# Performance work log

Measured on AMD Instinct MI355X. Metric: run time of the kernel, lower is better.

The kernel has to match this reference:

```python
import jax, jax.numpy as jnp
import numpy as np

T, B, D, H = 512, 64, 256, 512


def setup_inputs() -> dict:
    key = jax.random.key(0)
    k1, k2, k3, k4 = jax.random.split(key, 4)
    x = jax.random.normal(k1, (T, B, D), dtype=jnp.float32)
    should_reset = jax.random.randint(k2, (T, B), 0, 2, dtype=jnp.int32)
    # Linear([x, h]) -> 4H gates, Haiku/PyTorch-style fan-in init scale
    scale = 1.0 / np.sqrt(D + H)
    W = jax.random.normal(k3, (D + H, 4 * H), dtype=jnp.float32) * scale
    b = jax.random.normal(k4, (4 * H,), dtype=jnp.float32) * scale
    return {"x": x, "should_reset": should_reset, "W": W, "b": b}


def reference(x, should_reset, W, b):
    """ResetLSTM forward (reverse=False). x:[T,B,D], should_reset:[T,B] -> [T,B,H]."""
    h0 = jnp.zeros((x.shape[1], H), dtype=x.dtype)
    c0 = jnp.zeros((x.shape[1], H), dtype=x.dtype)
    reset = should_reset.astype(x.dtype)[..., None]  # [T,B,1]

    def step(carry, inp):
        h, c = carry
        xt, rt = inp
        keep = 1.0 - rt
        h = h * keep
        c = c * keep
        gates = jnp.concatenate([xt, h], axis=-1) @ W + b  # [B,4H]
        i, g, f, o = jnp.split(gates, 4, axis=-1)
        f = jax.nn.sigmoid(f + 1.0)  # Haiku forget bias +1
        i = jax.nn.sigmoid(i)
        g = jnp.tanh(g)
        o = jax.nn.sigmoid(o)
        new_c = f * c + i * g
        new_h = o * jnp.tanh(new_c)
        return (new_h, new_c), new_h

    _, outputs = jax.lax.scan(step, (h0, c0), (x, reset))
    return outputs  # [T,B,H]
```

## Files before the change

kernel.cpp:

```cpp
#include <hip/hip_runtime.h>

#define TSTEPS 512
#define BATCH  64
#define DIN    256
#define HID    512
#define NCH    8
#define VR     512
#define NRB    16
#define NUB    32
#define NWG    512
#define NTHR   256
#define HSST   520
#define GST    67

typedef __attribute__((ext_vector_type(8))) _Float16 f16x8;
typedef __attribute__((ext_vector_type(4))) _Float16 f16x4;
typedef __attribute__((ext_vector_type(4))) float f32x4;
typedef __attribute__((ext_vector_type(2))) float f32x2;

#define MFMA16(A,B,C) __builtin_amdgcn_mfma_f32_16x16x32_f16(A,B,C,0,0,0)
#define ALDU32(p) __hip_atomic_load(const_cast<unsigned*>(p), __ATOMIC_RELAXED, __HIP_MEMORY_SCOPE_AGENT)
#define ASTU32(p,v) __hip_atomic_store((p), (v), __ATOMIC_RELAXED, __HIP_MEMORY_SCOPE_AGENT)

__device__ __forceinline__ float sigm(float x) { return 1.0f / (1.0f + __expf(-x)); }

__device__ __forceinline__ void gld16_cc(f16x8& d, const void* p) {
  asm volatile("global_load_dwordx4 %0, %1, off sc0 sc1" : "=v"(d) : "v"(p));
}

__global__ void conv_x(const float* __restrict__ x, _Float16* __restrict__ xh, int n4) {
  int i = blockIdx.x * 256 + threadIdx.x;
  if (i >= n4) return;
  float4 v = reinterpret_cast<const float4*>(x)[i];
  f16x4 o;
  o[0] = (_Float16)v.x; o[1] = (_Float16)v.y; o[2] = (_Float16)v.z; o[3] = (_Float16)v.w;
  *reinterpret_cast<f16x4*>(xh + (size_t)i * 4) = o;
}

__global__ void w_prep(const float* __restrict__ W,
                       _Float16* __restrict__ WxT, _Float16* __restrict__ WhT) {
  int idx = blockIdx.x * 256 + threadIdx.x;
  if (idx < NUB * 64 * 256) {
    int k = idx & 255, cc = (idx >> 8) & 63, ub = idx >> 14;
    int unit = cc >> 2, g = cc & 3;
    int gcol = g * HID + ub * 16 + unit;
    WxT[idx] = (_Float16)W[k * 2048 + gcol];
  } else if (idx < NUB * 64 * 256 + NUB * 64 * 512) {
    int j = idx - NUB * 64 * 256;
    int k = j & 511, cc = (j >> 9) & 63, ub = j >> 15;
    int unit = cc >> 2, g = cc & 3;
    int gcol = g * HID + ub * 16 + unit;
    WhT[j] = (_Float16)W[(DIN + k) * 2048 + gcol];
  }
}

__global__ void seg_prep(const int* __restrict__ rst, int* __restrict__ tS,
                         int* __restrict__ segLen, int* __restrict__ maxLenB) {
  __shared__ int sMax[NRB];
  const int b = threadIdx.x;
  if (b < NRB) sMax[b] = 0;
  __syncthreads();
  int cut[NCH + 1];
  cut[0] = 0; cut[NCH] = TSTEPS;
  for (int c = 1; c < NCH; ++c) {
    int t = c * 64;
    while (t < TSTEPS && rst[t * BATCH + b] == 0) ++t;
    cut[c] = t;
  }
  for (int c = 1; c < NCH; ++c) if (cut[c] < cut[c - 1]) cut[c] = cut[c - 1];
  for (int c = 0; c < NCH; ++c) {
    int vr = c * 64 + b;
    tS[vr] = cut[c];
    int L = cut[c + 1] - cut[c];
    segLen[vr] = L;
    atomicMax(&sMax[c * 2 + (b >> 5)], L);
  }
  __syncthreads();
  if (b < NRB) maxLenB[b] = sMax[b];
}

__global__ void __launch_bounds__(NTHR, 2)
lstm_persistent(const _Float16* __restrict__ xh,
                const int* __restrict__ rst,
                const float* __restrict__ bias,
                float* __restrict__ out,
                unsigned long long* __restrict__ hb,
                unsigned* __restrict__ flags,
                const _Float16* __restrict__ WxT,
                const _Float16* __restrict__ WhT,
                const int* __restrict__ tS,
                const int* __restrict__ segLen,
                const int* __restrict__ maxLenB) {
  __shared__ _Float16 hS[32 * HSST];
  __shared__ float gateS[32 * GST];
  __shared__ float biasS[64];

  const int tid = threadIdx.x, wg = blockIdx.x;
  const int rb = wg >> 5, ub = wg & 31;
  const int vr0 = rb * 32;
  const int lane = tid & 63, wave = tid >> 6;
  const int colA = lane & 15, klo = (lane >> 4) * 8;

  f16x8 wx[8], wh[16];
  {
    const _Float16* px = WxT + ((size_t)ub * 64 + wave * 16 + colA) * 256 + klo;
    const _Float16* ph = WhT + ((size_t)ub * 64 + wave * 16 + colA) * 512 + klo;
#pragma unroll
    for (int ch = 0; ch < 8; ++ch) wx[ch] = *(const f16x8*)(px + ch * 32);
#pragma unroll
    for (int ch = 0; ch < 16; ++ch) wh[ch] = *(const f16x8*)(ph + ch * 32);
  }
  if (tid < 64) {
    int unit = tid >> 2, g = tid & 3;
    biasS[tid] = bias[g * HID + ub * 16 + unit];
  }

  int tSr0 = tS[vr0 + colA];
  int tSr1 = tS[vr0 + 16 + colA];

  const int crow = tid & 31, p = tid >> 5;
  const int vrc = vr0 + crow, bc = vrc & 63;
  const int tSc_ = tS[vrc], lenc_ = segLen[vrc];
  const int ML = maxLenB[rb];
  float cA = 0.f, cB = 0.f;

  __syncthreads();
  float bA[4], bB[4];
#pragma unroll
  for (int g = 0; g < 4; ++g) { bA[g] = biasS[8 * p + g]; bB[g] = biasS[8 * p + 4 + g]; }

  const int srow = tid >> 3, ss = tid & 7;

  for (int k = 0; k < ML; ++k) {
    f32x4 acc0 = {0.f, 0.f, 0.f, 0.f}, acc1 = {0.f, 0.f, 0.f, 0.f};
    {
      int t0 = tSr0 + k; if (t0 > TSTEPS - 1) t0 = TSTEPS - 1;
      int t1 = tSr1 + k; if (t1 > TSTEPS - 1) t1 = TSTEPS - 1;
      const int b0 = (vr0 + colA) & 63, b1 = (vr0 + 16 + colA) & 63;
      const _Float16* x0 = xh + ((size_t)t0 * BATCH + b0) * DIN + klo;
      const _Float16* x1 = xh + ((size_t)t1 * BATCH + b1) * DIN + klo;
#pragma unroll
      for (int ch = 0; ch < 8; ++ch) {
        f16x8 a0 = *(const f16x8*)(x0 + ch * 32);
        f16x8 a1 = *(const f16x8*)(x1 + ch * 32);
        acc0 = MFMA16(a0, wx[ch], acc0);
        acc1 = MFMA16(a1, wx[ch], acc1);
      }
    }

    if (k) {
      if (tid < NUB) {
        const unsigned tgt = (unsigned)k;
        while (ALDU32(flags + (rb * NUB + tid) * 16) < tgt) __builtin_amdgcn_s_sleep(1);
      }
      __syncthreads();
      asm volatile("" ::: "memory");

      {
        const char* hbase = (const char*)hb
            + (((size_t)(k & 1) * (VR * 128) + (size_t)(vr0 + srow) * 128) << 3)
            + ss * 16;
        f16x8 hq[8];
#pragma unroll
        for (int j = 0; j < 8; ++j) gld16_cc(hq[j], hbase + j * 128);
        asm volatile("s_waitcnt vmcnt(0)" ::: "memory");
        __builtin_amdgcn_sched_barrier(0);
#pragma unroll
        for (int j = 0; j < 8; ++j)
          *(f16x8*)&hS[srow * HSST + ss * 8 + j * 64] = hq[j];
      }
      __syncthreads();

#pragma unroll
      for (int ch = 0; ch < 16; ++ch) {
        f16x8 a0 = *(const f16x8*)&hS[colA * HSST + ch * 32 + klo];
        f16x8 a1 = *(const f16x8*)&hS[(16 + colA) * HSST + ch * 32 + klo];
        acc0 = MFMA16(a0, wh[ch], acc0);
        acc1 = MFMA16(a1, wh[ch], acc1);
      }
    }

#pragma unroll
    for (int rr = 0; rr < 4; ++rr) {
      int row0 = (lane >> 4) * 4 + rr;
      gateS[row0 * GST + wave * 16 + colA]        = acc0[rr];
      gateS[(16 + row0) * GST + wave * 16 + colA] = acc1[rr];
    }

    float hn0, hn1;
    {
      int kidx = tSc_ + k + 1; if (kidx > TSTEPS - 1) kidx = TSTEPS - 1;
      float keep = 1.0f - (float)rst[kidx * BATCH + bc];
      const float* g = &gateS[crow * GST + 8 * p];
      float i0 = sigm(g[0] + bA[0]);
      float t0 = tanhf(g[1] + bA[1]);
      float f0 = sigm(g[2] + bA[2] + 1.0f);
      float o0 = sigm(g[3] + bA[3]);
      float i1 = sigm(g[4] + bB[0]);
      float t1 = tanhf(g[5] + bB[1]);
      float f1 = sigm(g[6] + bB[2] + 1.0f);
      float o1 = sigm(g[7] + bB[3]);
      float cn0 = f0 * cA + i0 * t0, cn1 = f1 * cB + i1 * t1;
      hn0 = o0 * tanhf(cn0); hn1 = o1 * tanhf(cn1);
      cA = cn0 * keep; cB = cn1 * keep;
      if (k + 1 < ML) {
        union { _Float16 f[2]; unsigned u; } cv;
        cv.f[0] = (_Float16)(hn0 * keep);
        cv.f[1] = (_Float16)(hn1 * keep);
        unsigned* hb32 = (unsigned*)(hb + (size_t)((k + 1) & 1) * (VR * 128) + (size_t)vrc * 128);
        ASTU32(hb32 + ub * 8 + p, cv.u);
      }
    }

    __syncthreads();
    if (k + 1 < ML && tid == 0) ASTU32(flags + wg * 16, (unsigned)(k + 1));

    if (k < lenc_) {
      f32x2 o2 = {hn0, hn1};
      *(f32x2*)&out[((size_t)(tSc_ + k) * BATCH + bc) * HID + ub * 16 + 2 * p] = o2;
    }
  }
}

extern "C" void kernel_launch(void* const* d_in, const int* in_sizes, int n_in,
                              void* d_out, int out_size, void* d_ws, size_t ws_size,
                              hipStream_t stream) {
  const float* x   = (const float*)d_in[0];
  const int*   rst = (const int*)d_in[1];
  const float* W   = (const float*)d_in[2];
  const float* b   = (const float*)d_in[3];
  float* out = (float*)d_out;
  char* ws = (char*)d_ws;

  unsigned*           flags  = (unsigned*)(ws + 0);
  int*                tSp    = (int*)(ws + 32768);
  int*                segLen = (int*)(ws + 34816);
  int*                maxLenB= (int*)(ws + 36864);
  unsigned long long* hb     = (unsigned long long*)(ws + 40960);
  _Float16*           xh     = (_Float16*)(ws + 40960 + 1048576);
  _Float16*           WxT    = (_Float16*)(ws + 40960 + 1048576 + 16777216);
  _Float16*           WhT    = (_Float16*)(ws + 40960 + 1048576 + 16777216 + 1048576);

  hipMemsetAsync(ws, 0, 32768, stream);

  int n4 = TSTEPS * BATCH * DIN / 4;
  hipLaunchKernelGGL(conv_x, dim3(n4 / 256), dim3(256), 0, stream, x, xh, n4);
  hipLaunchKernelGGL(w_prep, dim3(6144), dim3(256), 0, stream, W, WxT, WhT);
  hipLaunchKernelGGL(seg_prep, dim3(1), dim3(64), 0, stream, rst, tSp, segLen, maxLenB);

  hipLaunchKernelGGL(lstm_persistent, dim3(NWG), dim3(NTHR), 0, stream,
                     xh, rst, b, out, hb, flags, WxT, WhT, tSp, segLen, maxLenB);
}
```

Measured before the change: 505.7 us.

## Balance reset-segment split, remap workgroups by XCC, use L2-scope h exchange

Segment cutting now binary-searches the smallest maximum chunk length, so each batch row's 8 chunks are balanced and the number of sequential steps (ML) can shrink. Workgroups are renumbered so the 32 unit-blocks sharing a row-block are strided by 16. At startup each workgroup records its XCC id; if all its partners share an XCC, the hidden-state exchange uses sc0 (L2-coherent) loads and stores instead of system-coherent ones, which cuts per-step communication latency. This adds a startup handshake and depends on the hardware dispatching the workgroups onto the same XCC, otherwise it falls back to the old path.

```diff
diff --git a/kernel.cpp b/kernel.cpp
--- a/kernel.cpp
+++ b/kernel.cpp
@@ -26,6 +26,12 @@
 
 __device__ __forceinline__ void gld16_cc(f16x8& d, const void* p) {
   asm volatile("global_load_dwordx4 %0, %1, off sc0 sc1" : "=v"(d) : "v"(p));
+}
+__device__ __forceinline__ void gld16_l2(f16x8& d, const void* p) {
+  asm volatile("global_load_dwordx4 %0, %1, off sc0" : "=v"(d) : "v"(p));
+}
+__device__ __forceinline__ void gld16_pin(f16x8& d, const void* p) {
+  asm volatile("global_load_dwordx4 %0, %1, off" : "=v"(d) : "v"(p));
 }
 
 __global__ void conv_x(const float* __restrict__ x, _Float16* __restrict__ xh, int n4) {
@@ -60,20 +66,34 @@
   const int b = threadIdx.x;
   if (b < NRB) sMax[b] = 0;
   __syncthreads();
-  int cut[NCH + 1];
-  cut[0] = 0; cut[NCH] = TSTEPS;
-  for (int c = 1; c < NCH; ++c) {
-    int t = c * 64;
-    while (t < TSTEPS && rst[t * BATCH + b] == 0) ++t;
-    cut[c] = t;
-  }
-  for (int c = 1; c < NCH; ++c) if (cut[c] < cut[c - 1]) cut[c] = cut[c - 1];
+  int lo = (TSTEPS + NCH - 1) / NCH, hi = TSTEPS;
+  while (lo < hi) {
+    int L = (lo + hi) >> 1;
+    int pos = 0; bool ok = false;
+    for (int s = 0; s < NCH; ++s) {
+      int target = pos + L;
+      if (target >= TSTEPS) { ok = true; break; }
+      int t = target;
+      while (t > pos && rst[t * BATCH + b] == 0) --t;
+      if (t == pos) break;
+      pos = t;
+    }
+    if (ok) hi = L; else lo = L + 1;
+  }
+  const int L = lo;
+  int pos = 0;
   for (int c = 0; c < NCH; ++c) {
+    int start = pos, end = pos;
+    if (pos < TSTEPS) {
+      int target = pos + L;
+      if (target >= TSTEPS) end = TSTEPS;
+      else { int t = target; while (t > pos && rst[t * BATCH + b] == 0) --t; end = t; }
+      pos = end;
+    }
     int vr = c * 64 + b;
-    tS[vr] = cut[c];
-    int L = cut[c + 1] - cut[c];
-    segLen[vr] = L;
-    atomicMax(&sMax[c * 2 + (b >> 5)], L);
+    tS[vr] = start;
+    segLen[vr] = end - start;
+    atomicMax(&sMax[c * 2 + (b >> 5)], end - start);
   }
   __syncthreads();
   if (b < NRB) maxLenB[b] = sMax[b];
@@ -86,6 +106,7 @@
                 float* __restrict__ out,
                 unsigned long long* __restrict__ hb,
                 unsigned* __restrict__ flags,
+                unsigned* __restrict__ xccb,
                 const _Float16* __restrict__ WxT,
                 const _Float16* __restrict__ WhT,
                 const int* __restrict__ tS,
@@ -94,21 +115,40 @@
   __shared__ _Float16 hS[32 * HSST];
   __shared__ float gateS[32 * GST];
   __shared__ float biasS[64];
+  __shared__ int uniformS;
 
   const int tid = threadIdx.x, wg = blockIdx.x;
-  const int rb = wg >> 5, ub = wg & 31;
+  const int ub = wg >> 4;
+  const int rb = ((wg & 7) << 1) | ((wg >> 3) & 1);
+  const int wgbase = wg & 15;
   const int vr0 = rb * 32;
   const int lane = tid & 63, wave = tid >> 6;
   const int colA = lane & 15, klo = (lane >> 4) * 8;
+
+  unsigned myxcc;
+  asm volatile("s_getreg_b32 %0, hwreg(HW_REG_XCC_ID)" : "=s"(myxcc));
+  if (tid == 0) {
+    uniformS = 1;
+    ASTU32(xccb + wg * 16, 0x100u | (myxcc & 0xffu));
+  }
+  __syncthreads();
+  if (tid < NUB) {
+    int mwg = (tid << 4) | wgbase;
+    unsigned v;
+    do { v = ALDU32(xccb + mwg * 16); if (!v) __builtin_amdgcn_s_sleep(1); } while (!v);
+    if ((v & 0xffu) != (myxcc & 0xffu)) uniformS = 0;
+  }
 
   f16x8 wx[8], wh[16];
   {
     const _Float16* px = WxT + ((size_t)ub * 64 + wave * 16 + colA) * 256 + klo;
     const _Float16* ph = WhT + ((size_t)ub * 64 + wave * 16 + colA) * 512 + klo;
 #pragma unroll
-    for (int ch = 0; ch < 8; ++ch) wx[ch] = *(const f16x8*)(px + ch * 32);
-#pragma unroll
-    for (int ch = 0; ch < 16; ++ch) wh[ch] = *(const f16x8*)(ph + ch * 32);
+    for (int ch = 0; ch < 8; ++ch) gld16_pin(wx[ch], px + ch * 32);
+#pragma unroll
+    for (int ch = 0; ch < 16; ++ch) gld16_pin(wh[ch], ph + ch * 32);
+    asm volatile("s_waitcnt vmcnt(0)" ::: "memory");
+    __builtin_amdgcn_sched_barrier(0);
   }
   if (tid < 64) {
     int unit = tid >> 2, g = tid & 3;
@@ -125,6 +165,7 @@
   float cA = 0.f, cB = 0.f;
 
   __syncthreads();
+  const bool useL2 = (uniformS != 0);
   float bA[4], bB[4];
 #pragma unroll
   for (int g = 0; g < 4; ++g) { bA[g] = biasS[8 * p + g]; bB[g] = biasS[8 * p + 4 + g]; }
@@ -151,7 +192,8 @@
     if (k) {
       if (tid < NUB) {
         const unsigned tgt = (unsigned)k;
-        while (ALDU32(flags + (rb * NUB + tid) * 16) < tgt) __builtin_amdgcn_s_sleep(1);
+        while (ALDU32(flags + ((tid << 4) | wgbase) * 16) < tgt)
+          __builtin_amdgcn_s_sleep(1);
       }
       __syncthreads();
       asm volatile("" ::: "memory");
@@ -161,8 +203,13 @@
             + (((size_t)(k & 1) * (VR * 128) + (size_t)(vr0 + srow) * 128) << 3)
             + ss * 16;
         f16x8 hq[8];
-#pragma unroll
-        for (int j = 0; j < 8; ++j) gld16_cc(hq[j], hbase + j * 128);
+        if (useL2) {
+#pragma unroll
+          for (int j = 0; j < 8; ++j) gld16_l2(hq[j], hbase + j * 128);
+        } else {
+#pragma unroll
+          for (int j = 0; j < 8; ++j) gld16_cc(hq[j], hbase + j * 128);
+        }
         asm volatile("s_waitcnt vmcnt(0)" ::: "memory");
         __builtin_amdgcn_sched_barrier(0);
 #pragma unroll
@@ -207,8 +254,12 @@
         union { _Float16 f[2]; unsigned u; } cv;
         cv.f[0] = (_Float16)(hn0 * keep);
         cv.f[1] = (_Float16)(hn1 * keep);
-        unsigned* hb32 = (unsigned*)(hb + (size_t)((k + 1) & 1) * (VR * 128) + (size_t)vrc * 128);
-        ASTU32(hb32 + ub * 8 + p, cv.u);
+        unsigned* dst = (unsigned*)(hb + (size_t)((k + 1) & 1) * (VR * 128)
+                                       + (size_t)vrc * 128) + ub * 8 + p;
+        if (useL2)
+          asm volatile("global_store_dword %0, %1, off sc0" :: "v"(dst), "v"(cv.u) : "memory");
+        else
+          ASTU32(dst, cv.u);
       }
     }
 
@@ -233,15 +284,16 @@
   char* ws = (char*)d_ws;
 
   unsigned*           flags  = (unsigned*)(ws + 0);
-  int*                tSp    = (int*)(ws + 32768);
-  int*                segLen = (int*)(ws + 34816);
-  int*                maxLenB= (int*)(ws + 36864);
-  unsigned long long* hb     = (unsigned long long*)(ws + 40960);
-  _Float16*           xh     = (_Float16*)(ws + 40960 + 1048576);
-  _Float16*           WxT    = (_Float16*)(ws + 40960 + 1048576 + 16777216);
-  _Float16*           WhT    = (_Float16*)(ws + 40960 + 1048576 + 16777216 + 1048576);
-
-  hipMemsetAsync(ws, 0, 32768, stream);
+  unsigned*           xccb   = (unsigned*)(ws + 32768);
+  int*                tSp    = (int*)(ws + 65536);
+  int*                segLen = (int*)(ws + 67584);
+  int*                maxLenB= (int*)(ws + 69632);
+  unsigned long long* hb     = (unsigned long long*)(ws + 73728);
+  _Float16*           xh     = (_Float16*)(ws + 73728 + 1048576);
+  _Float16*           WxT    = (_Float16*)(ws + 73728 + 1048576 + 16777216);
+  _Float16*           WhT    = (_Float16*)(ws + 73728 + 1048576 + 16777216 + 1048576);
+
+  hipMemsetAsync(ws, 0, 65536, stream);
 
   int n4 = TSTEPS * BATCH * DIN / 4;
   hipLaunchKernelGGL(conv_x, dim3(n4 / 256), dim3(256), 0, stream, x, xh, n4);
@@ -249,5 +301,5 @@
   hipLaunchKernelGGL(seg_prep, dim3(1), dim3(64), 0, stream, rst, tSp, segLen, maxLenB);
 
   hipLaunchKernelGGL(lstm_persistent, dim3(NWG), dim3(NTHR), 0, stream,
-                     xh, rst, b, out, hb, flags, WxT, WhT, tSp, segLen, maxLenB);
-}
+                     xh, rst, b, out, hb, flags, xccb, WxT, WhT, tSp, segLen, maxLenB);
+}
```

After: 544.7 us. +7.7%, slower.
